# Optimization experiments

Measured on AMD Instinct MI355X. Metric: run time of the kernel, lower is better.

The kernel has to match this reference:

```python
import jax, jax.numpy as jnp
import numpy as np

B, N, IN_DIM, H, D = 2, 4096, 64, 4, 32
NEG_SLOPE = 0.1
NEG_INF = -9e15


def setup_inputs() -> dict:
    key = jax.random.key(0)
    ks = jax.random.split(key, 9)
    vt = jax.random.normal(ks[0], (1,), dtype=jnp.float32)
    x = jax.random.normal(ks[1], (B, N, IN_DIM), dtype=jnp.float32)
    adj = jax.random.randint(ks[2], (N, N), 0, 2).astype(jnp.float32)
    # xavier-uniform-ish scales
    g = float(np.sqrt(2.0))  # relu gain
    lim_fc = g * np.sqrt(6.0 / (IN_DIM + H * D))
    lim_p = g * np.sqrt(6.0 / (D + D))
    fc_w = jax.random.uniform(ks[3], (H * D, IN_DIM), jnp.float32, -lim_fc, lim_fc)
    fc_b = jnp.zeros((H * D,), jnp.float32)
    Q1 = jax.random.uniform(ks[4], (H, D, D), jnp.float32, -lim_p, lim_p)
    Q2 = jax.random.uniform(ks[5], (H, D, D), jnp.float32, -lim_p, lim_p)
    K = jax.random.uniform(ks[6], (H, D, D), jnp.float32, -lim_p, lim_p)
    V = jax.random.uniform(ks[7], (H, D, D), jnp.float32, -lim_p, lim_p)
    return {"vt": vt, "x": x, "adj": adj, "fc_w": fc_w, "fc_b": fc_b,
            "Q1": Q1, "Q2": Q2, "K": K, "V": V}


def _leaky(a):
    return jnp.where(a >= 0, a, NEG_SLOPE * a)


def reference(vt, x, adj, fc_w, fc_b, Q1, Q2, K, V):
    b, n, _ = x.shape
    h, d, _ = Q1.shape
    # per-head projection: [B,N,in] -> [B,H,N,d]
    xp = (x @ fc_w.T + fc_b).reshape(b, n, h, d).transpose(0, 2, 1, 3)
    Qt1 = jnp.einsum('bhnd,hde->bhne', xp, Q1)
    Qt2 = jnp.einsum('bhnd,hde->bhne', xp, Q2)
    Kt = jnp.einsum('bhnd,hde->bhne', xp, K)
    Vt = jnp.einsum('bhnd,hde->bhne', xp, V)
    Qt = _leaky(Qt1 + Qt2)
    QKt = _leaky(jnp.einsum('bhnd,bhmd->bhnm', Qt, Kt))  # [B,H,N,N]
    AQKt = adj * QKt                                      # adj broadcasts [N,N]
    AQKt = jnp.where(AQKt == 0, NEG_INF, AQKt)
    attn = jax.nn.softmax(AQKt, axis=-1)
    rst = jnp.einsum('bhnm,bhmd->bhnd', attn, Vt).transpose(0, 2, 1, 3)  # [B,N,H,d]
    return jax.nn.relu(rst)
```

## Files before the change

kernel.cpp:

```cpp
#include <hip/hip_runtime.h>
#include <hip/hip_bf16.h>

#define NEG_SLOPE_C 0.1f
#define LOG2E_C 1.4426950408889634f
#define NEGB_C (-1.3e16f)

constexpr int B_ = 2, N_ = 4096, IN_ = 64, H_ = 4, D_ = 32;

typedef float f32x16 __attribute__((ext_vector_type(16)));
typedef __bf16 bf16x8 __attribute__((ext_vector_type(8)));

__device__ inline unsigned short f2bfu(float x) {
    unsigned u = __float_as_uint(x);
    return (unsigned short)((u + 0x7fffu + ((u >> 16) & 1u)) >> 16);
}
__device__ inline float bfu2f(unsigned short s) { return __uint_as_float(((unsigned)s) << 16); }
__device__ inline bf16x8 ld_bf8(const unsigned short* p) {
    uint4 r = *reinterpret_cast<const uint4*>(p);
    return __builtin_bit_cast(bf16x8, r);
}

__global__ __launch_bounds__(256) void prep_fcT(const float* __restrict__ fc_w,
                                                float* __restrict__ fc_wT) {
    int t = blockIdx.x * 256 + threadIdx.x;
    int c = t >> 6, k = t & 63;
    fc_wT[k * 128 + c] = fc_w[c * 64 + k];
}

__global__ __launch_bounds__(256) void pack_adjT(const float* __restrict__ adj,
                                                 unsigned* __restrict__ maskT) {
    const int g = blockIdx.x * 4 + (threadIdx.x >> 6);
    const int lane = threadIdx.x & 63;
    const int qg = g >> 6;
    const int mc = g & 63;
    const float* ap = adj + (size_t)qg * 32 * N_ + mc * 64 + lane;
    unsigned word = 0;
    #pragma unroll
    for (int i = 0; i < 32; ++i) {
        unsigned long long ball = __ballot(ap[(size_t)i * N_] != 0.0f);
        word |= (unsigned)((ball >> lane) & 1ULL) << i;
    }
    maskT[(size_t)qg * N_ + mc * 64 + lane] = word;
}

__global__ __launch_bounds__(128) void proj_kernel(
    const float* __restrict__ x, const float* __restrict__ fc_wT,
    const float* __restrict__ fc_b, const float* __restrict__ Q1,
    const float* __restrict__ Q2, const float* __restrict__ K,
    const float* __restrict__ V,
    unsigned short* __restrict__ QtH, unsigned short* __restrict__ QtL,
    unsigned short* __restrict__ KtH, unsigned short* __restrict__ KtL,
    unsigned short* __restrict__ Vt) {
    const int t = threadIdx.x;
    const int h = t >> 5, e = t & 31;
    const float* q1p = Q1 + h * D_ * D_;
    const float* q2p = Q2 + h * D_ * D_;
    const float* kp  = K  + h * D_ * D_;
    const float* vp  = V  + h * D_ * D_;
    __shared__ float xr[IN_];
    __shared__ float xp[H_ * D_];
    const float bias = fc_b[t];
    for (int rr = 0; rr < 8; ++rr) {
        const int bn = blockIdx.x * 8 + rr;
        const int b = bn / N_, n = bn % N_;
        if (t < IN_) xr[t] = x[(long long)bn * IN_ + t];
        __syncthreads();
        float acc = bias;
        #pragma unroll
        for (int k = 0; k < IN_; ++k) acc += xr[k] * fc_wT[k * 128 + t];
        xp[t] = acc;
        __syncthreads();
        const float* xph = xp + h * D_;
        float a1 = 0.f, a2 = 0.f, ak = 0.f, av = 0.f;
        #pragma unroll
        for (int d = 0; d < D_; ++d) {
            float xv = xph[d];
            a1 += xv * q1p[d * D_ + e];
            a2 += xv * q2p[d * D_ + e];
            ak += xv * kp [d * D_ + e];
            av += xv * vp [d * D_ + e];
        }
        float q = a1 + a2;
        q = q >= 0.f ? q : NEG_SLOPE_C * q;
        size_t o = ((size_t)(b * H_ + h) * N_ + n) * D_ + e;
        unsigned short qh = f2bfu(q);
        QtH[o] = qh;
        QtL[o] = f2bfu(q - bfu2f(qh));
        unsigned short kh = f2bfu(ak);
        KtH[o] = kh;
        KtL[o] = f2bfu(ak - bfu2f(kh));
        Vt[o]  = f2bfu(av);
        __syncthreads();
    }
}

__global__ __launch_bounds__(256) void vtrans(const unsigned short* __restrict__ Vt,
                                              unsigned short* __restrict__ VtT) {
    const int bh = blockIdx.x >> 6;
    const int n0 = (blockIdx.x & 63) * 64;
    __shared__ unsigned short tile[64][34];
    const int t = threadIdx.x;
    {
        const int r = t >> 2, c = (t & 3) * 8;
        uint4 v = *reinterpret_cast<const uint4*>(Vt + ((size_t)bh * N_ + n0 + r) * D_ + c);
        *reinterpret_cast<uint4*>(&tile[r][c]) = v;
    }
    __syncthreads();
    {
        const int d = t >> 3, nc = (t & 7) * 8;
        unsigned short tmp[8];
        #pragma unroll
        for (int j = 0; j < 8; ++j) tmp[j] = tile[nc + j][d];
        *reinterpret_cast<uint4*>(VtT + ((size_t)bh * D_ + d) * N_ + n0 + nc) =
            *reinterpret_cast<uint4*>(tmp);
    }
}

__global__ __launch_bounds__(512, 6) void flash_mfma(
    const unsigned short* __restrict__ QtH, const unsigned short* __restrict__ QtL,
    const unsigned short* __restrict__ KtH, const unsigned short* __restrict__ KtL,
    const unsigned short* __restrict__ VtT, const unsigned* __restrict__ maskT,
    float* __restrict__ out) {
    const int bid = blockIdx.x;
    const int bh = bid >> 7;
    const int qg = bid & 127;
    const int b = bh >> 2, h = bh & 3;
    const int t = threadIdx.x;
    const int w = t >> 6;
    const int wu = __builtin_amdgcn_readfirstlane(w);
    const int l = t & 63;
    const int lq = l & 31;
    const int hi = l >> 5;
    const int q0 = qg * 32;

    const size_t bhND = (size_t)bh * N_ * D_;
    const unsigned short* qbh = QtH + bhND + (size_t)(q0 + lq) * D_ + hi * 8;
    const unsigned short* qbl = QtL + bhND + (size_t)(q0 + lq) * D_ + hi * 8;
    const bf16x8 qh0 = ld_bf8(qbh), qh1 = ld_bf8(qbh + 16);
    const bf16x8 ql0 = ld_bf8(qbl), ql1 = ld_bf8(qbl + 16);

    f32x16 acc = {};
    float m_run = -3.0e38f, l_run = 0.f;
    const float negb = NEGB_C;
    const float C1 = 0.55f * LOG2E_C, C2 = 0.45f * LOG2E_C;

    const int kw0 = wu * 512;
    const unsigned short* kh_p = KtH + bhND + (size_t)(kw0 + lq) * D_ + hi * 8;
    const unsigned short* kl_p = KtL + bhND + (size_t)(kw0 + lq) * D_ + hi * 8;
    const unsigned short* v_p  = VtT + ((size_t)bh * D_ + lq) * N_ + kw0 + hi * 8;
    const unsigned* mp = maskT + (size_t)qg * N_ + wu * 512;

    for (int tt = 0; tt < 16; ++tt) {
        unsigned mwd[32];
        {
            const uint4* mq = reinterpret_cast<const uint4*>(mp + tt * 32);
            #pragma unroll
            for (int i = 0; i < 8; ++i) {
                uint4 v = mq[i];
                mwd[i*4] = v.x; mwd[i*4+1] = v.y; mwd[i*4+2] = v.z; mwd[i*4+3] = v.w;
            }
        }
        const bf16x8 kh0v = ld_bf8(kh_p), kh1v = ld_bf8(kh_p + 16);
        const bf16x8 kl0v = ld_bf8(kl_p), kl1v = ld_bf8(kl_p + 16);
        const bf16x8 v0   = ld_bf8(v_p),  v1   = ld_bf8(v_p + 16);
        kh_p += 32 * D_; kl_p += 32 * D_; v_p += 32;

        f32x16 s = {};
        s = __builtin_amdgcn_mfma_f32_32x32x16_bf16(kh0v, qh0, s, 0, 0, 0);
        s = __builtin_amdgcn_mfma_f32_32x32x16_bf16(kh1v, qh1, s, 0, 0, 0);
        s = __builtin_amdgcn_mfma_f32_32x32x16_bf16(kh0v, ql0, s, 0, 0, 0);
        s = __builtin_amdgcn_mfma_f32_32x32x16_bf16(kh1v, ql1, s, 0, 0, 0);
        s = __builtin_amdgcn_mfma_f32_32x32x16_bf16(kl0v, qh0, s, 0, 0, 0);
        s = __builtin_amdgcn_mfma_f32_32x32x16_bf16(kl1v, qh1, s, 0, 0, 0);

        float am[16];
        #pragma unroll
        for (int r = 0; r < 16; ++r) {
            const int j0 = (r & 3) + 8 * (r >> 2);
            const unsigned long long msk =
                (unsigned long long)mwd[j0] | ((unsigned long long)mwd[j0 + 4] << 32);
            const float v = s[r];
            const float a = fmaf(C2, fabsf(v), C1 * v);
            asm("v_cndmask_b32 %0, %1, %2, %3"
                : "=v"(am[r]) : "v"(negb), "v"(a), "s"(msk));
        }
        const float x0 = fmaxf(fmaxf(am[0], am[1]), am[2]);
        const float x1 = fmaxf(fmaxf(am[3], am[4]), am[5]);
        const float x2 = fmaxf(fmaxf(am[6], am[7]), am[8]);
        const float x3 = fmaxf(fmaxf(am[9], am[10]), am[11]);
        const float x4 = fmaxf(fmaxf(am[12], am[13]), am[14]);
        const float y0 = fmaxf(fmaxf(x0, x1), x2);
        const float y1 = fmaxf(fmaxf(x3, x4), am[15]);
        float cmax = fmaxf(y0, y1);
        cmax = fmaxf(cmax, __shfl_xor(cmax, 32));
        if (!__all(cmax <= m_run)) {
            const float nm = fmaxf(m_run, cmax);
            const float sc = __builtin_amdgcn_exp2f(m_run - nm);
            l_run *= sc;
            #pragma unroll
            for (int r = 0; r < 16; ++r) acc[r] *= sc;
            m_run = nm;
        }
        float e[16];
        #pragma unroll
        for (int r = 0; r < 16; ++r) e[r] = __builtin_amdgcn_exp2f(am[r] - m_run);
        const float s0 = (e[0] + e[1]) + (e[2] + e[3]);
        const float s1 = (e[4] + e[5]) + (e[6] + e[7]);
        const float s2 = (e[8] + e[9]) + (e[10] + e[11]);
        const float s3 = (e[12] + e[13]) + (e[14] + e[15]);
        float lsum = (s0 + s1) + (s2 + s3);
        lsum += __shfl_xor(lsum, 32);
        l_run += lsum;
        unsigned c0w, c1w, c2w, c3w, c4w, c5w, c6w, c7w;
        asm("v_cvt_pk_bf16_f32 %0, %1, %2" : "=v"(c0w) : "v"(e[0]),  "v"(e[1]));
        asm("v_cvt_pk_bf16_f32 %0, %1, %2" : "=v"(c1w) : "v"(e[2]),  "v"(e[3]));
        asm("v_cvt_pk_bf16_f32 %0, %1, %2" : "=v"(c2w) : "v"(e[4]),  "v"(e[5]));
        asm("v_cvt_pk_bf16_f32 %0, %1, %2" : "=v"(c3w) : "v"(e[6]),  "v"(e[7]));
        asm("v_cvt_pk_bf16_f32 %0, %1, %2" : "=v"(c4w) : "v"(e[8]),  "v"(e[9]));
        asm("v_cvt_pk_bf16_f32 %0, %1, %2" : "=v"(c5w) : "v"(e[10]), "v"(e[11]));
        asm("v_cvt_pk_bf16_f32 %0, %1, %2" : "=v"(c6w) : "v"(e[12]), "v"(e[13]));
        asm("v_cvt_pk_bf16_f32 %0, %1, %2" : "=v"(c7w) : "v"(e[14]), "v"(e[15]));
        asm("v_permlane32_swap_b32 %0, %1" : "+v"(c0w), "+v"(c2w));
        asm("v_permlane32_swap_b32 %0, %1" : "+v"(c1w), "+v"(c3w));
        asm("v_permlane32_swap_b32 %0, %1" : "+v"(c4w), "+v"(c6w));
        asm("v_permlane32_swap_b32 %0, %1" : "+v"(c5w), "+v"(c7w));
        const uint4 b0u = make_uint4(c0w, c1w, c2w, c3w);
        const uint4 b1u = make_uint4(c4w, c5w, c6w, c7w);
        acc = __builtin_amdgcn_mfma_f32_32x32x16_bf16(v0, __builtin_bit_cast(bf16x8, b0u), acc, 0, 0, 0);
        acc = __builtin_amdgcn_mfma_f32_32x32x16_bf16(v1, __builtin_bit_cast(bf16x8, b1u), acc, 0, 0, 0);
    }

    __shared__ float o_lds[8][32][33];
    __shared__ float m_l[8][32];
    __shared__ float l_l[8][32];
    if (hi == 0) { m_l[w][lq] = m_run; l_l[w][lq] = l_run; }
    #pragma unroll
    for (int r = 0; r < 16; ++r) {
        const int d = (r & 3) + 8 * (r >> 2) + 4 * hi;
        o_lds[w][d][lq] = acc[r];
    }
    __syncthreads();
    {
        const int q = t >> 4;
        const int dp = t & 15;
        float M = m_l[0][q];
        #pragma unroll
        for (int w2 = 1; w2 < 8; ++w2) M = fmaxf(M, m_l[w2][q]);
        float L = 0.f, fac[8];
        #pragma unroll
        for (int w2 = 0; w2 < 8; ++w2) {
            fac[w2] = __builtin_amdgcn_exp2f(m_l[w2][q] - M);
            L += l_l[w2][q] * fac[w2];
        }
        const float invL = 1.f / L;
        float o0 = 0.f, o1 = 0.f;
        #pragma unroll
        for (int w2 = 0; w2 < 8; ++w2) {
            o0 += o_lds[w2][dp * 2][q] * fac[w2];
            o1 += o_lds[w2][dp * 2 + 1][q] * fac[w2];
        }
        o0 = fmaxf(o0 * invL, 0.f);
        o1 = fmaxf(o1 * invL, 0.f);
        float2 ov = make_float2(o0, o1);
        *reinterpret_cast<float2*>(out + ((size_t)(b * N_ + q0 + q) * H_ + h) * D_ + dp * 2) = ov;
    }
}

extern "C" void kernel_launch(void* const* d_in, const int* in_sizes, int n_in,
                              void* d_out, int out_size, void* d_ws, size_t ws_size,
                              hipStream_t stream) {
    const float* x    = (const float*)d_in[1];
    const float* adj  = (const float*)d_in[2];
    const float* fc_w = (const float*)d_in[3];
    const float* fc_b = (const float*)d_in[4];
    const float* Q1   = (const float*)d_in[5];
    const float* Q2   = (const float*)d_in[6];
    const float* K    = (const float*)d_in[7];
    const float* V    = (const float*)d_in[8];
    float* out = (float*)d_out;

    char* ws = (char*)d_ws;
    const size_t MB = 1024 * 1024;
    unsigned short* QtH = (unsigned short*)(ws);
    unsigned short* QtL = (unsigned short*)(ws + 2 * MB);
    unsigned short* KtH = (unsigned short*)(ws + 4 * MB);
    unsigned short* KtL = (unsigned short*)(ws + 6 * MB);
    unsigned short* Vt  = (unsigned short*)(ws + 8 * MB);
    unsigned short* VtT = (unsigned short*)(ws + 10 * MB);
    unsigned*     maskT = (unsigned*)    (ws + 12 * MB);
    float*        fc_wT = (float*)       (ws + 14 * MB);

    hipLaunchKernelGGL(prep_fcT, dim3(32), dim3(256), 0, stream, fc_w, fc_wT);
    hipLaunchKernelGGL(pack_adjT, dim3(2048), dim3(256), 0, stream, adj, maskT);
    hipLaunchKernelGGL(proj_kernel, dim3(B_ * N_ / 8), dim3(128), 0, stream,
                       x, fc_wT, fc_b, Q1, Q2, K, V, QtH, QtL, KtH, KtL, Vt);
    hipLaunchKernelGGL(vtrans, dim3(8 * (N_ / 64)), dim3(256), 0, stream, Vt, VtT);
    hipLaunchKernelGGL(flash_mfma, dim3(B_ * H_ * (N_ / 32)), dim3(512), 0, stream,
                       QtH, QtL, KtH, KtL, VtT, maskT, out);
}
```

Measured before the change: 105.3 us.

## Use row-major adjacency bitmask and split keys across four waves per block

The adjacency packing now writes a plain row-major bitmask with one coalesced ballot per 64 elements, replacing the transposed packing. The attention kernel reads one mask word per lane per tile and selects per element with shifts and a conditional, instead of building SGPR lane masks from uniform loads. Blocks shrink from 8 to 4 waves, each covering 1024 keys over 32 iterations, and the cross-wave merge is reduced to match. This lowers packing cost and merge overhead, but adds per-element VALU work, strided per-lane mask loads and fewer waves in flight to hide latency.

```diff
diff --git a/kernel.cpp b/kernel.cpp
--- a/kernel.cpp
+++ b/kernel.cpp
@@ -27,20 +27,14 @@
     fc_wT[k * 128 + c] = fc_w[c * 64 + k];
 }
 
-__global__ __launch_bounds__(256) void pack_adjT(const float* __restrict__ adj,
-                                                 unsigned* __restrict__ maskT) {
-    const int g = blockIdx.x * 4 + (threadIdx.x >> 6);
-    const int lane = threadIdx.x & 63;
-    const int qg = g >> 6;
-    const int mc = g & 63;
-    const float* ap = adj + (size_t)qg * 32 * N_ + mc * 64 + lane;
-    unsigned word = 0;
-    #pragma unroll
-    for (int i = 0; i < 32; ++i) {
-        unsigned long long ball = __ballot(ap[(size_t)i * N_] != 0.0f);
-        word |= (unsigned)((ball >> lane) & 1ULL) << i;
-    }
-    maskT[(size_t)qg * N_ + mc * 64 + lane] = word;
+__global__ __launch_bounds__(256) void pack_adj(const float* __restrict__ adj,
+                                                unsigned* __restrict__ maskbits) {
+    long long idx = (long long)blockIdx.x * blockDim.x + threadIdx.x;
+    float a = adj[idx];
+    unsigned long long ball = __ballot(a != 0.0f);
+    int lane = threadIdx.x & 63;
+    if (lane == 0)       maskbits[idx >> 5] = (unsigned)(ball & 0xffffffffULL);
+    else if (lane == 32) maskbits[idx >> 5] = (unsigned)(ball >> 32);
 }
 
 __global__ __launch_bounds__(128) void proj_kernel(
@@ -116,10 +110,10 @@
     }
 }
 
-__global__ __launch_bounds__(512, 6) void flash_mfma(
+__global__ __launch_bounds__(256, 8) void flash_mfma(
     const unsigned short* __restrict__ QtH, const unsigned short* __restrict__ QtL,
     const unsigned short* __restrict__ KtH, const unsigned short* __restrict__ KtL,
-    const unsigned short* __restrict__ VtT, const unsigned* __restrict__ maskT,
+    const unsigned short* __restrict__ VtT, const unsigned* __restrict__ maskb,
     float* __restrict__ out) {
     const int bid = blockIdx.x;
     const int bh = bid >> 7;
@@ -144,22 +138,15 @@
     const float negb = NEGB_C;
     const float C1 = 0.55f * LOG2E_C, C2 = 0.45f * LOG2E_C;
 
-    const int kw0 = wu * 512;
+    const int kw0 = wu * 1024;
     const unsigned short* kh_p = KtH + bhND + (size_t)(kw0 + lq) * D_ + hi * 8;
     const unsigned short* kl_p = KtL + bhND + (size_t)(kw0 + lq) * D_ + hi * 8;
     const unsigned short* v_p  = VtT + ((size_t)bh * D_ + lq) * N_ + kw0 + hi * 8;
-    const unsigned* mp = maskT + (size_t)qg * N_ + wu * 512;
-
-    for (int tt = 0; tt < 16; ++tt) {
-        unsigned mwd[32];
-        {
-            const uint4* mq = reinterpret_cast<const uint4*>(mp + tt * 32);
-            #pragma unroll
-            for (int i = 0; i < 8; ++i) {
-                uint4 v = mq[i];
-                mwd[i*4] = v.x; mwd[i*4+1] = v.y; mwd[i*4+2] = v.z; mwd[i*4+3] = v.w;
-            }
-        }
+    const unsigned* mrow = maskb + (size_t)(q0 + lq) * (N_ / 32) + wu * 32;
+
+    for (int tt = 0; tt < 32; ++tt) {
+        const unsigned word = mrow[tt];
+        const unsigned word_h = word >> (hi * 4);
         const bf16x8 kh0v = ld_bf8(kh_p), kh1v = ld_bf8(kh_p + 16);
         const bf16x8 kl0v = ld_bf8(kl_p), kl1v = ld_bf8(kl_p + 16);
         const bf16x8 v0   = ld_bf8(v_p),  v1   = ld_bf8(v_p + 16);
@@ -176,13 +163,10 @@
         float am[16];
         #pragma unroll
         for (int r = 0; r < 16; ++r) {
-            const int j0 = (r & 3) + 8 * (r >> 2);
-            const unsigned long long msk =
-                (unsigned long long)mwd[j0] | ((unsigned long long)mwd[j0 + 4] << 32);
+            const int sh = (r & 3) + 8 * (r >> 2);
             const float v = s[r];
             const float a = fmaf(C2, fabsf(v), C1 * v);
-            asm("v_cndmask_b32 %0, %1, %2, %3"
-                : "=v"(am[r]) : "v"(negb), "v"(a), "s"(msk));
+            am[r] = ((word_h >> sh) & 1u) ? a : negb;
         }
         const float x0 = fmaxf(fmaxf(am[0], am[1]), am[2]);
         const float x1 = fmaxf(fmaxf(am[3], am[4]), am[5]);
@@ -230,9 +214,9 @@
         acc = __builtin_amdgcn_mfma_f32_32x32x16_bf16(v1, __builtin_bit_cast(bf16x8, b1u), acc, 0, 0, 0);
     }
 
-    __shared__ float o_lds[8][32][33];
-    __shared__ float m_l[8][32];
-    __shared__ float l_l[8][32];
+    __shared__ float o_lds[4][32][33];
+    __shared__ float m_l[4][32];
+    __shared__ float l_l[4][32];
     if (hi == 0) { m_l[w][lq] = m_run; l_l[w][lq] = l_run; }
     #pragma unroll
     for (int r = 0; r < 16; ++r) {
@@ -241,28 +225,27 @@
     }
     __syncthreads();
     {
-        const int q = t >> 4;
-        const int dp = t & 15;
-        float M = m_l[0][q];
-        #pragma unroll
-        for (int w2 = 1; w2 < 8; ++w2) M = fmaxf(M, m_l[w2][q]);
-        float L = 0.f, fac[8];
-        #pragma unroll
-        for (int w2 = 0; w2 < 8; ++w2) {
+        const int q = t & 31;
+        const int d2 = t >> 5;
+        const float M = fmaxf(fmaxf(m_l[0][q], m_l[1][q]), fmaxf(m_l[2][q], m_l[3][q]));
+        float L = 0.f, fac[4];
+        #pragma unroll
+        for (int w2 = 0; w2 < 4; ++w2) {
             fac[w2] = __builtin_amdgcn_exp2f(m_l[w2][q] - M);
             L += l_l[w2][q] * fac[w2];
         }
         const float invL = 1.f / L;
-        float o0 = 0.f, o1 = 0.f;
-        #pragma unroll
-        for (int w2 = 0; w2 < 8; ++w2) {
-            o0 += o_lds[w2][dp * 2][q] * fac[w2];
-            o1 += o_lds[w2][dp * 2 + 1][q] * fac[w2];
-        }
-        o0 = fmaxf(o0 * invL, 0.f);
-        o1 = fmaxf(o1 * invL, 0.f);
-        float2 ov = make_float2(o0, o1);
-        *reinterpret_cast<float2*>(out + ((size_t)(b * N_ + q0 + q) * H_ + h) * D_ + dp * 2) = ov;
+        float ov[4];
+        #pragma unroll
+        for (int j = 0; j < 4; ++j) {
+            const int d = d2 * 4 + j;
+            float o = 0.f;
+            #pragma unroll
+            for (int w2 = 0; w2 < 4; ++w2) o += o_lds[w2][d][q] * fac[w2];
+            ov[j] = fmaxf(o * invL, 0.f);
+        }
+        float4 o4 = make_float4(ov[0], ov[1], ov[2], ov[3]);
+        *reinterpret_cast<float4*>(out + ((size_t)(b * N_ + q0 + q) * H_ + h) * D_ + d2 * 4) = o4;
     }
 }
 
@@ -287,14 +270,14 @@
     unsigned short* KtL = (unsigned short*)(ws + 6 * MB);
     unsigned short* Vt  = (unsigned short*)(ws + 8 * MB);
     unsigned short* VtT = (unsigned short*)(ws + 10 * MB);
-    unsigned*     maskT = (unsigned*)    (ws + 12 * MB);
+    unsigned*     maskb = (unsigned*)    (ws + 12 * MB);
     float*        fc_wT = (float*)       (ws + 14 * MB);
 
     hipLaunchKernelGGL(prep_fcT, dim3(32), dim3(256), 0, stream, fc_w, fc_wT);
-    hipLaunchKernelGGL(pack_adjT, dim3(2048), dim3(256), 0, stream, adj, maskT);
+    hipLaunchKernelGGL(pack_adj, dim3(N_ * N_ / 256), dim3(256), 0, stream, adj, maskb);
     hipLaunchKernelGGL(proj_kernel, dim3(B_ * N_ / 8), dim3(128), 0, stream,
                        x, fc_wT, fc_b, Q1, Q2, K, V, QtH, QtL, KtH, KtL, Vt);
     hipLaunchKernelGGL(vtrans, dim3(8 * (N_ / 64)), dim3(256), 0, stream, Vt, VtT);
-    hipLaunchKernelGGL(flash_mfma, dim3(B_ * H_ * (N_ / 32)), dim3(512), 0, stream,
-                       QtH, QtL, KtH, KtL, VtT, maskT, out);
-}
+    hipLaunchKernelGGL(flash_mfma, dim3(B_ * H_ * (N_ / 32)), dim3(256), 0, stream,
+                       QtH, QtL, KtH, KtL, VtT, maskb, out);
+}
```

After: 169.3 us. 1.61x slower.

## Repack adjacency mask per query row and software-pipeline K loads in flash loop

Applied to the files above, without the earlier changes.

The adjacency bitmask is repacked so each lane reads one 32-bit word per 32-key tile for its own query row, rather than loading 32 transposed words per tile into registers. The flash loop is unrolled by two with double-buffered K tiles and mask words prefetched one iteration ahead, so global loads overlap the QK MFMAs and the softmax. Occupancy hint drops from 6 to 4 waves to leave room for the extra registers. The new pack kernel does fully coalesced reads over adj but launches many more small blocks, and the mask select becomes a per-element bit test instead of an SGPR cndmask.

```diff
diff --git a/kernel.cpp b/kernel.cpp
--- a/kernel.cpp
+++ b/kernel.cpp
@@ -27,20 +27,23 @@
     fc_wT[k * 128 + c] = fc_w[c * 64 + k];
 }
 
-__global__ __launch_bounds__(256) void pack_adjT(const float* __restrict__ adj,
-                                                 unsigned* __restrict__ maskT) {
-    const int g = blockIdx.x * 4 + (threadIdx.x >> 6);
-    const int lane = threadIdx.x & 63;
-    const int qg = g >> 6;
-    const int mc = g & 63;
-    const float* ap = adj + (size_t)qg * 32 * N_ + mc * 64 + lane;
-    unsigned word = 0;
-    #pragma unroll
-    for (int i = 0; i < 32; ++i) {
-        unsigned long long ball = __ballot(ap[(size_t)i * N_] != 0.0f);
-        word |= (unsigned)((ball >> lane) & 1ULL) << i;
-    }
-    maskT[(size_t)qg * N_ + mc * 64 + lane] = word;
+__global__ __launch_bounds__(256) void pack_adjL(const float* __restrict__ adj,
+                                                 unsigned* __restrict__ maskL) {
+    long long idx = (long long)blockIdx.x * blockDim.x + threadIdx.x;
+    float a = adj[idx];
+    unsigned long long ball = __ballot(a != 0.0f);
+    int lane = threadIdx.x & 63;
+    unsigned word = 0; bool wr = false;
+    if (lane == 0)       { word = (unsigned)(ball & 0xffffffffULL); wr = true; }
+    else if (lane == 32) { word = (unsigned)(ball >> 32);           wr = true; }
+    if (wr) {
+        const long long widx = idx >> 5;
+        const int q  = (int)(widx >> 7);
+        const int kc = (int)(widx & 127);
+        const int qg = q >> 5, lq = q & 31;
+        const int strip = kc >> 4, tt = kc & 15;
+        maskL[(((size_t)(qg * 8 + strip) * 16) + tt) * 32 + lq] = word;
+    }
 }
 
 __global__ __launch_bounds__(128) void proj_kernel(
@@ -116,10 +119,10 @@
     }
 }
 
-__global__ __launch_bounds__(512, 6) void flash_mfma(
+__global__ __launch_bounds__(512, 4) void flash_mfma(
     const unsigned short* __restrict__ QtH, const unsigned short* __restrict__ QtL,
     const unsigned short* __restrict__ KtH, const unsigned short* __restrict__ KtL,
-    const unsigned short* __restrict__ VtT, const unsigned* __restrict__ maskT,
+    const unsigned short* __restrict__ VtT, const unsigned* __restrict__ maskL,
     float* __restrict__ out) {
     const int bid = blockIdx.x;
     const int bh = bid >> 7;
@@ -148,41 +151,30 @@
     const unsigned short* kh_p = KtH + bhND + (size_t)(kw0 + lq) * D_ + hi * 8;
     const unsigned short* kl_p = KtL + bhND + (size_t)(kw0 + lq) * D_ + hi * 8;
     const unsigned short* v_p  = VtT + ((size_t)bh * D_ + lq) * N_ + kw0 + hi * 8;
-    const unsigned* mp = maskT + (size_t)qg * N_ + wu * 512;
-
-    for (int tt = 0; tt < 16; ++tt) {
-        unsigned mwd[32];
-        {
-            const uint4* mq = reinterpret_cast<const uint4*>(mp + tt * 32);
-            #pragma unroll
-            for (int i = 0; i < 8; ++i) {
-                uint4 v = mq[i];
-                mwd[i*4] = v.x; mwd[i*4+1] = v.y; mwd[i*4+2] = v.z; mwd[i*4+3] = v.w;
-            }
-        }
-        const bf16x8 kh0v = ld_bf8(kh_p), kh1v = ld_bf8(kh_p + 16);
-        const bf16x8 kl0v = ld_bf8(kl_p), kl1v = ld_bf8(kl_p + 16);
-        const bf16x8 v0   = ld_bf8(v_p),  v1   = ld_bf8(v_p + 16);
-        kh_p += 32 * D_; kl_p += 32 * D_; v_p += 32;
-
+    const unsigned* ml_p = maskL + ((size_t)(qg * 8 + wu) * 16) * 32 + lq;
+
+    auto qk6 = [&](const bf16x8& a0, const bf16x8& a1,
+                   const bf16x8& b0, const bf16x8& b1) -> f32x16 {
         f32x16 s = {};
-        s = __builtin_amdgcn_mfma_f32_32x32x16_bf16(kh0v, qh0, s, 0, 0, 0);
-        s = __builtin_amdgcn_mfma_f32_32x32x16_bf16(kh1v, qh1, s, 0, 0, 0);
-        s = __builtin_amdgcn_mfma_f32_32x32x16_bf16(kh0v, ql0, s, 0, 0, 0);
-        s = __builtin_amdgcn_mfma_f32_32x32x16_bf16(kh1v, ql1, s, 0, 0, 0);
-        s = __builtin_amdgcn_mfma_f32_32x32x16_bf16(kl0v, qh0, s, 0, 0, 0);
-        s = __builtin_amdgcn_mfma_f32_32x32x16_bf16(kl1v, qh1, s, 0, 0, 0);
-
+        s = __builtin_amdgcn_mfma_f32_32x32x16_bf16(a0, qh0, s, 0, 0, 0);
+        s = __builtin_amdgcn_mfma_f32_32x32x16_bf16(a1, qh1, s, 0, 0, 0);
+        s = __builtin_amdgcn_mfma_f32_32x32x16_bf16(a0, ql0, s, 0, 0, 0);
+        s = __builtin_amdgcn_mfma_f32_32x32x16_bf16(a1, ql1, s, 0, 0, 0);
+        s = __builtin_amdgcn_mfma_f32_32x32x16_bf16(b0, qh0, s, 0, 0, 0);
+        s = __builtin_amdgcn_mfma_f32_32x32x16_bf16(b1, qh1, s, 0, 0, 0);
+        return s;
+    };
+
+    auto softpv = [&](const f32x16& s, unsigned word) {
+        const bf16x8 v0 = ld_bf8(v_p), v1 = ld_bf8(v_p + 16); v_p += 32;
+        const unsigned word_h = word >> (hi * 4);
         float am[16];
         #pragma unroll
         for (int r = 0; r < 16; ++r) {
-            const int j0 = (r & 3) + 8 * (r >> 2);
-            const unsigned long long msk =
-                (unsigned long long)mwd[j0] | ((unsigned long long)mwd[j0 + 4] << 32);
-            const float v = s[r];
-            const float a = fmaf(C2, fabsf(v), C1 * v);
-            asm("v_cndmask_b32 %0, %1, %2, %3"
-                : "=v"(am[r]) : "v"(negb), "v"(a), "s"(msk));
+            const int sh = (r & 3) + 8 * (r >> 2);
+            const float vv = s[r];
+            const float aa = fmaf(C2, fabsf(vv), C1 * vv);
+            am[r] = ((word_h >> sh) & 1u) ? aa : negb;
         }
         const float x0 = fmaxf(fmaxf(am[0], am[1]), am[2]);
         const float x1 = fmaxf(fmaxf(am[3], am[4]), am[5]);
@@ -228,6 +220,32 @@
         const uint4 b1u = make_uint4(c4w, c5w, c6w, c7w);
         acc = __builtin_amdgcn_mfma_f32_32x32x16_bf16(v0, __builtin_bit_cast(bf16x8, b0u), acc, 0, 0, 0);
         acc = __builtin_amdgcn_mfma_f32_32x32x16_bf16(v1, __builtin_bit_cast(bf16x8, b1u), acc, 0, 0, 0);
+    };
+
+    bf16x8 Akh0 = ld_bf8(kh_p), Akh1 = ld_bf8(kh_p + 16);
+    bf16x8 Akl0 = ld_bf8(kl_p), Akl1 = ld_bf8(kl_p + 16);
+    unsigned Amw = ml_p[0];
+    kh_p += 32 * D_; kl_p += 32 * D_;
+    bf16x8 Bkh0 = ld_bf8(kh_p), Bkh1 = ld_bf8(kh_p + 16);
+    bf16x8 Bkl0 = ld_bf8(kl_p), Bkl1 = ld_bf8(kl_p + 16);
+    unsigned Bmw = ml_p[32];
+    kh_p += 32 * D_; kl_p += 32 * D_;
+
+    for (int it = 0; it < 8; ++it) {
+        const unsigned mwE = Amw;
+        const f32x16 sE = qk6(Akh0, Akh1, Akl0, Akl1);
+        Akh0 = ld_bf8(kh_p); Akh1 = ld_bf8(kh_p + 16);
+        Akl0 = ld_bf8(kl_p); Akl1 = ld_bf8(kl_p + 16);
+        Amw  = ml_p[(2 * it + 2) * 32];
+        kh_p += 32 * D_; kl_p += 32 * D_;
+        softpv(sE, mwE);
+        const unsigned mwO = Bmw;
+        const f32x16 sO = qk6(Bkh0, Bkh1, Bkl0, Bkl1);
+        Bkh0 = ld_bf8(kh_p); Bkh1 = ld_bf8(kh_p + 16);
+        Bkl0 = ld_bf8(kl_p); Bkl1 = ld_bf8(kl_p + 16);
+        Bmw  = ml_p[(2 * it + 3) * 32];
+        kh_p += 32 * D_; kl_p += 32 * D_;
+        softpv(sO, mwO);
     }
 
     __shared__ float o_lds[8][32][33];
@@ -287,14 +305,14 @@
     unsigned short* KtL = (unsigned short*)(ws + 6 * MB);
     unsigned short* Vt  = (unsigned short*)(ws + 8 * MB);
     unsigned short* VtT = (unsigned short*)(ws + 10 * MB);
-    unsigned*     maskT = (unsigned*)    (ws + 12 * MB);
+    unsigned*     maskL = (unsigned*)    (ws + 12 * MB);
     float*        fc_wT = (float*)       (ws + 14 * MB);
 
     hipLaunchKernelGGL(prep_fcT, dim3(32), dim3(256), 0, stream, fc_w, fc_wT);
-    hipLaunchKernelGGL(pack_adjT, dim3(2048), dim3(256), 0, stream, adj, maskT);
+    hipLaunchKernelGGL(pack_adjL, dim3(N_ * N_ / 256), dim3(256), 0, stream, adj, maskL);
     hipLaunchKernelGGL(proj_kernel, dim3(B_ * N_ / 8), dim3(128), 0, stream,
                        x, fc_wT, fc_b, Q1, Q2, K, V, QtH, QtL, KtH, KtL, Vt);
     hipLaunchKernelGGL(vtrans, dim3(8 * (N_ / 64)), dim3(256), 0, stream, Vt, VtT);
     hipLaunchKernelGGL(flash_mfma, dim3(B_ * H_ * (N_ / 32)), dim3(512), 0, stream,
-                       QtH, QtL, KtH, KtL, VtT, maskT, out);
-}
+                       QtH, QtL, KtH, KtL, VtT, maskL, out);
+}
```

After: 123.4 us. 1.17x slower.
